# Performance work log

Measured on AMD Instinct MI355X. Metric: run time of the kernel, lower is better.

The kernel has to match this reference:

```python
import jax, jax.numpy as jnp
import numpy as np

B, T, N, DG = 4, 24, 2048, 64
E, H, W, P, NH = 128, 64, 64, 8, 4
HD = E // NH
HP, WP = H // P, W // P
NP = HP * WP
SCALE = float(np.sqrt(HD))


def _mlp(x, w1, b1, w2, b2):
    return jax.nn.relu(x @ w1 + b1) @ w2 + b2


def _interp_linear(x, out_len):
    # x: (B, L, C); linear interpolation along L to out_len, align_corners=False (PyTorch semantics)
    L = x.shape[1]
    src = jnp.maximum((jnp.arange(out_len, dtype=jnp.float32) + 0.5) * (L / out_len) - 0.5, 0.0)
    i0 = jnp.floor(src).astype(jnp.int32)
    lam = (src - i0.astype(jnp.float32))[None, :, None]
    i1 = jnp.minimum(i0 + 1, L - 1)
    return x[:, i0] * (1.0 - lam) + x[:, i1] * lam


def _cross_attn(Q, K, V, qw, qb, kw, kb, vw, vb, ow, ob):
    b, ql, _ = Q.shape
    kl = K.shape[1]
    q = (Q @ qw + qb).reshape(b, ql, NH, HD).transpose(0, 2, 1, 3)
    k = (K @ kw + kb).reshape(b, kl, NH, HD).transpose(0, 2, 1, 3)
    v = (V @ vw + vb).reshape(b, kl, NH, HD).transpose(0, 2, 1, 3)
    s = jnp.einsum('bhqd,bhkd->bhqk', q, k) / SCALE
    a = jax.nn.softmax(s, axis=-1)
    o = jnp.einsum('bhqk,bhkd->bhqd', a, v).transpose(0, 2, 1, 3).reshape(b, ql, E)
    o = o @ ow + ob
    # permute -> F.interpolate(size=k_len, mode='linear') -> permute back
    return _interp_linear(o, kl)


def _forward(graph_features, grid_features, graph_time_indices, grid_time_indices,
             gek_w1, gek_b1, gek_w2, gek_b2, gev_w1, gev_b1, gev_w2, gev_b2,
             rk_w1, rk_b1, rk_w2, rk_b2, rv_w1, rv_b1, rv_w2, rv_b2,
             te_w1, te_b1, te_w2, te_b2, pe_w, pe_b, up_w, up_b,
             ag_q_w, ag_q_b, ag_k_w, ag_k_b, ag_v_w, ag_v_b, ag_o_w, ag_o_b,
             ar_q_w, ar_q_b, ar_k_w, ar_k_b, ar_v_w, ar_v_b, ar_o_w, ar_o_b):
    # time embedding (query), q_len = T
    te = _mlp(graph_time_indices[:, :, None], te_w1, te_b1, te_w2, te_b2)  # (B, T, E)
    # graph branch
    gf = graph_features.reshape(B, T * N, DG)
    gk = _mlp(gf, gek_w1, gek_b1, gek_w2, gek_b2)
    gv = _mlp(gf, gev_w1, gev_b1, gev_w2, gev_b2)
    g_out = _cross_attn(te, gk, gv, ag_q_w, ag_q_b, ag_k_w, ag_k_b, ag_v_w, ag_v_b, ag_o_w, ag_o_b)
    g_out = g_out.reshape(B, T, N, E)
    # grid branch: non-overlapping patch conv (kernel=stride=P) as einsum
    xp = grid_features.reshape(B * T, E, HP, P, WP, P)
    patches = jnp.einsum('bchpwq,ocpq->bhwo', xp, pe_w) + pe_b  # (BT, HP, WP, E)
    patches = patches.reshape(B, T * NP, E)
    rk = _mlp(patches, rk_w1, rk_b1, rk_w2, rk_b2)
    rv = _mlp(patches, rv_w1, rv_b1, rv_w2, rv_b2)
    r_out = _cross_attn(te, rk, rv, ar_q_w, ar_q_b, ar_k_w, ar_k_b, ar_v_w, ar_v_b, ar_o_w, ar_o_b)  # (B, T*NP, E)
    r = r_out.reshape(B * T, HP, WP, E)
    # ConvTranspose2d with kernel=stride=P: each pixel expands to a PxP block
    up = jnp.einsum('bijc,copq->boipjq', r, up_w).reshape(B * T, E, H, W) + up_b[None, :, None, None]
    return g_out, up.reshape(B, T, E, H, W)


def setup_inputs():
    key = jax.random.key(0)
    ks = iter(jax.random.split(key, 64))
    def mk(shape):
        return jax.random.normal(next(ks), shape, dtype=jnp.float32) * 0.02
    d = {}
    d['graph_features'] = jax.random.normal(next(ks), (B, T, N, DG), dtype=jnp.float32)
    d['grid_features'] = jax.random.normal(next(ks), (B, T, E, H, W), dtype=jnp.float32)
    d['graph_time_indices'] = jax.random.uniform(next(ks), (B, T), dtype=jnp.float32)
    d['grid_time_indices'] = jax.random.uniform(next(ks), (B, T), dtype=jnp.float32)
    for pfx, din in (('gek', DG), ('gev', DG), ('rk', E), ('rv', E), ('te', 1)):
        d[pfx + '_w1'] = mk((din, E)); d[pfx + '_b1'] = jnp.zeros((E,), jnp.float32)
        d[pfx + '_w2'] = mk((E, E)); d[pfx + '_b2'] = jnp.zeros((E,), jnp.float32)
    d['pe_w'] = mk((E, E, P, P)); d['pe_b'] = jnp.zeros((E,), jnp.float32)
    d['up_w'] = mk((E, E, P, P)); d['up_b'] = jnp.zeros((E,), jnp.float32)
    for pfx in ('ag', 'ar'):
        for nm in ('q', 'k', 'v', 'o'):
            d[pfx + '_' + nm + '_w'] = mk((E, E)); d[pfx + '_' + nm + '_b'] = jnp.zeros((E,), jnp.float32)
    return d


def reference(graph_features, grid_features, graph_time_indices, grid_time_indices,
              gek_w1, gek_b1, gek_w2, gek_b2, gev_w1, gev_b1, gev_w2, gev_b2,
              rk_w1, rk_b1, rk_w2, rk_b2, rv_w1, rv_b1, rv_w2, rv_b2,
              te_w1, te_b1, te_w2, te_b2, pe_w, pe_b, up_w, up_b,
              ag_q_w, ag_q_b, ag_k_w, ag_k_b, ag_v_w, ag_v_b, ag_o_w, ag_o_b,
              ar_q_w, ar_q_b, ar_k_w, ar_k_b, ar_v_w, ar_v_b, ar_o_w, ar_o_b):
    return _forward(graph_features, grid_features, graph_time_indices, grid_time_indices,
                    gek_w1, gek_b1, gek_w2, gek_b2, gev_w1, gev_b1, gev_w2, gev_b2,
                    rk_w1, rk_b1, rk_w2, rk_b2, rv_w1, rv_b1, rv_w2, rv_b2,
                    te_w1, te_b1, te_w2, te_b2, pe_w, pe_b, up_w, up_b,
                    ag_q_w, ag_q_b, ag_k_w, ag_k_b, ag_v_w, ag_v_b, ag_o_w, ag_o_b,
                    ar_q_w, ar_q_b, ar_k_w, ar_k_b, ar_v_w, ar_v_b, ar_o_w, ar_o_b)
```

## Files before the change

### kernel.cpp

```cpp
#include <hip/hip_runtime.h>


typedef unsigned short u16;
using bf8 = __attribute__((ext_vector_type(8))) short;
using f4v = __attribute__((ext_vector_type(4))) float;
#define MFMA16(a, b, c) __builtin_amdgcn_mfma_f32_16x16x32_bf16(a, b, c, 0, 0, 0)

constexpr float INV_SCALE = 0.17677669529663687f;

__device__ __forceinline__ u16 f2bf(float f) {
  unsigned u = __float_as_uint(f);
  u += 0x7FFFu + ((u >> 16) & 1u);
  return (u16)(u >> 16);
}
__device__ __forceinline__ unsigned pk2(float a, float b) {
  return (unsigned)f2bf(a) | ((unsigned)f2bf(b) << 16);
}
__device__ __forceinline__ float bflo(unsigned v) { return __uint_as_float(v << 16); }
__device__ __forceinline__ float bfhi(unsigned v) { return __uint_as_float(v & 0xffff0000u); }


__global__ __launch_bounds__(128) void k_pre1(
    const float* gk_w1, const float* gv_w1, const float* rk_w1, const float* rv_w1,
    u16* W1c_g, u16* W1c_r,
    const float* pe_w, u16* peB,
    const float* tidx, const float* te_w1, const float* te_b1,
    const float* te_w2, const float* te_b2,
    const float* wg, const float* bg, const float* wr, const float* br,
    float* qg, float* qr,
    const float* A0, const float* Ab0, const float* B0, const float* Bb0, float* O0, float* Ob0,
    const float* A1, const float* Ab1, const float* B1, const float* Bb1, float* O1, float* Ob1,
    const float* A2, const float* Ab2, const float* B2, const float* Bb2, float* O2, float* Ob2,
    const float* A3, const float* Ab3, const float* B3, const float* Bb3, float* O3, float* Ob3) {
  int x = blockIdx.x, e = threadIdx.x;
  __shared__ float sh[256];
  if (x < 512) {
    int c = x & 255, brn = x >> 8;
    int DIN = brn ? 128 : 64;
    if (e < DIN) {
      const float* src = brn ? (c < 128 ? rk_w1 : rv_w1) : (c < 128 ? gk_w1 : gv_w1);
      u16* dst = brn ? W1c_r : W1c_g;
      dst[c * DIN + e] = f2bf(src[e * 128 + (c & 127)]);
    }
  } else if (x < 1536) {
    int i = ((x - 512) * 128 + e) * 8;
    float4 v0 = *(const float4*)(pe_w + i);
    float4 v1 = *(const float4*)(pe_w + i + 4);
    uint4 o; o.x = pk2(v0.x, v0.y); o.y = pk2(v0.z, v0.w);
    o.z = pk2(v1.x, v1.y); o.w = pk2(v1.z, v1.w);
    *(uint4*)&peB[i] = o;
  } else if (x < 1632) {
    int row = x - 1536;
    float tv = tidx[row];
    sh[e] = fmaxf(tv * te_w1[e] + te_b1[e], 0.f);
    __syncthreads();
    float a = te_b2[e];
    for (int j = 0; j < 128; ++j) a += sh[j] * te_w2[j * 128 + e];
    sh[128 + e] = a;
    __syncthreads();
    float ag = bg[e], ar = br[e];
    for (int j = 0; j < 128; ++j) {
      float xx = sh[128 + j];
      ag += xx * wg[j * 128 + e];
      ar += xx * wr[j * 128 + e];
    }
    qg[row * 128 + e] = ag;
    qr[row * 128 + e] = ar;
  } else {
    int sub = x - 1632;
    int task = sub / 129, j = sub % 129;
    const float *A, *Ab, *Bm, *Bb; float *O, *Ob;
    switch (task) {
      case 0: A=A0; Ab=Ab0; Bm=B0; Bb=Bb0; O=O0; Ob=Ob0; break;
      case 1: A=A1; Ab=Ab1; Bm=B1; Bb=Bb1; O=O1; Ob=Ob1; break;
      case 2: A=A2; Ab=Ab2; Bm=B2; Bb=Bb2; O=O2; Ob=Ob2; break;
      default:A=A3; Ab=Ab3; Bm=B3; Bb=Bb3; O=O3; Ob=Ob3; break;
    }
    sh[e] = (j < 128) ? A[j * 128 + e] : Ab[e];
    __syncthreads();
    float acc = (j < 128) ? 0.f : Bb[e];
    for (int m = 0; m < 128; ++m) acc += sh[m] * Bm[m * 128 + e];
    if (j < 128) O[j * 128 + e] = acc; else Ob[e] = acc;
  }
}


__global__ __launch_bounds__(128) void k_wvopk(
    const float* Wv_g, const float* bv_g, const float* ow_g, const float* ob_g, float* Wvo_g, float* bvo_g,
    const float* Wv_r, const float* bv_r, const float* ow_r, const float* ob_r, float* Wvo_r, float* bvo_r,
    const float* Wk_g, const float* bk_g, const float* q_g, u16* PkT_g, float* ck_g,
    const float* Wk_r, const float* bk_r, const float* q_r, u16* PkT_r, float* ck_r) {
  int j = blockIdx.x, e = threadIdx.x;
  if (blockIdx.y < 8) {
    int br = blockIdx.y >> 2, h = blockIdx.y & 3;
    const float* Wv = br ? Wv_r : Wv_g;  const float* bv = br ? bv_r : bv_g;
    const float* ow = br ? ow_r : ow_g;  const float* ob = br ? ob_r : ob_g;
    float* Wvo = br ? Wvo_r : Wvo_g;     float* bvo = br ? bvo_r : bvo_g;
    if (j < 128) {
      __shared__ float wrow[32];
      if (e < 32) wrow[e] = Wv[j * 128 + h * 32 + e];
      __syncthreads();
      float acc = 0.f;
      for (int d = 0; d < 32; ++d) acc += wrow[d] * ow[(h * 32 + d) * 128 + e];
      Wvo[(h * 128 + j) * 128 + e] = acc;
    } else if (h == 0) {
      __shared__ float bbv[128];
      bbv[e] = bv[e];
      __syncthreads();
      float acc = ob[e];
      for (int m = 0; m < 128; ++m) acc += bbv[m] * ow[m * 128 + e];
      bvo[e] = acc;
    }
  } else {
    int y = blockIdx.y - 8;
    int br = y >> 2, b = y & 3;
    int hq = e;
    if (hq >= 96) return;
    const float* Wk = br ? Wk_r : Wk_g;  const float* bk = br ? bk_r : bk_g;
    const float* q  = br ? q_r  : q_g;
    u16* PkT = br ? PkT_r : PkT_g;       float* ck = br ? ck_r : ck_g;
    int h = hq / 24, t = hq % 24;
    const float* qrow = q + (b * 24 + t) * 128 + h * 32;
    if (j < 128) {
      const float* wrow = Wk + j * 128 + h * 32;
      float acc = 0.f;
      for (int d = 0; d < 32; ++d) acc += wrow[d] * qrow[d];
      PkT[((size_t)b * 96 + hq) * 136 + j] = f2bf(acc * INV_SCALE);
    } else {
      float acc = 0.f;
      for (int d = 0; d < 32; ++d) acc += bk[h * 32 + d] * qrow[d];
      ck[b * 96 + hq] = acc * INV_SCALE;
    }
  }
}


template <int DIN, int NRED, bool INBF>
__device__ __forceinline__ void flash_body(char* smem,
    const void* __restrict__ Xv, const float* __restrict__ redbias, size_t rstride,
    const u16* __restrict__ W1c, const float* __restrict__ b1k, const float* __restrict__ b1v,
    const u16* __restrict__ PkT, const float* __restrict__ ck,
    u16* __restrict__ accP, float* __restrict__ lP,
    int KL, int kpb, int chunk, int b, int nchunk) {
  constexpr int KS = DIN / 32;
  constexpr int PD = DIN + 8;
  constexpr int PH = 136, PV = 72, PP = 72;
  constexpr int NR = DIN / 16;
  constexpr int XTN = 64 * PD;
  u16* Xt   = (u16*)smem;
  u16* HB   = (u16*)(smem + 4 * XTN);
  u16* Pt   = (u16*)(smem + 4 * XTN + 18432);
  u16* Pk_s = (u16*)(smem + 4 * XTN + 18432 + 13824);
  float* lred = (float*)(smem + 4 * XTN + 18432 + 13824 + 26112);

  int t = threadIdx.x;
  int l = t & 63, w = t >> 6;
  int l16 = l & 15, l4 = l >> 4;

  size_t xbase = (size_t)b * KL * DIN + (size_t)chunk * kpb * DIN;

  {
    const unsigned* ps = (const unsigned*)(PkT + (size_t)b * 96 * 136);
    unsigned* pd = (unsigned*)Pk_s;
    for (int i = t; i < 96 * 136 / 2; i += 256) pd[i] = ps[i];
  }

  bf8 wkA[2][KS], wvB[2][KS];
#pragma unroll
  for (int m = 0; m < 2; ++m)
#pragma unroll
    for (int ks = 0; ks < KS; ++ks) {
      int hid = w * 32 + m * 16 + l16;
      wkA[m][ks] = *(const bf8*)(W1c + (size_t)hid * DIN + ks * 32 + l4 * 8);
      wvB[m][ks] = *(const bf8*)(W1c + (size_t)(128 + hid) * DIN + ks * 32 + l4 * 8);
    }
  float bkA[2][4], bvB[2], ckr[6];
#pragma unroll
  for (int m = 0; m < 2; ++m)
#pragma unroll
    for (int r = 0; r < 4; ++r) bkA[m][r] = b1k[w * 32 + m * 16 + l4 * 4 + r];
#pragma unroll
  for (int n = 0; n < 2; ++n) bvB[n] = b1v[w * 32 + n * 16 + l16];
#pragma unroll
  for (int n = 0; n < 6; ++n) ckr[n] = ck[b * 96 + n * 16 + l16];

  f4v accO[6][2];
#pragma unroll
  for (int m = 0; m < 6; ++m)
#pragma unroll
    for (int n = 0; n < 2; ++n) accO[m][n] = (f4v){0.f, 0.f, 0.f, 0.f};
  float lacc[6] = {0.f, 0.f, 0.f, 0.f, 0.f, 0.f};

  float4 xr[NR];
  auto load_tile = [&](int kt) {
#pragma unroll
    for (int r = 0; r < NR; ++r) {
      int idx = (r * 256 + t) * 4;
      if constexpr (!INBF) {
        const float* Xrow = (const float*)Xv + xbase + (size_t)kt * 64 * DIN;
        xr[r] = *(const float4*)(Xrow + idx);
      } else {
        const u16* Xrow = (const u16*)Xv + xbase + (size_t)kt * 64 * DIN;
        int din = idx % DIN;
        float4 a = *(const float4*)(redbias + din);
#pragma unroll
        for (int c = 0; c < NRED; ++c) {
          uint2 v = *(const uint2*)(Xrow + (size_t)c * rstride + idx);
          a.x += bflo(v.x); a.y += bfhi(v.x);
          a.z += bflo(v.y); a.w += bfhi(v.y);
        }
        xr[r] = a;
      }
    }
  };

  int ntile = kpb >> 6;
  load_tile(0);
  int buf = 0;
  for (int kt = 0; kt < ntile; ++kt) {
#pragma unroll
    for (int r = 0; r < NR; ++r) {
      int idx = (r * 256 + t) * 4;
      int key = idx / DIN, din = idx % DIN;
      uint2 o; o.x = pk2(xr[r].x, xr[r].y); o.y = pk2(xr[r].z, xr[r].w);
      *(uint2*)&Xt[buf * XTN + key * PD + din] = o;
    }
    if (kt + 1 < ntile) load_tile(kt + 1);
    __syncthreads();

    {
      f4v hk[2][4];
#pragma unroll
      for (int m = 0; m < 2; ++m)
#pragma unroll
        for (int n = 0; n < 4; ++n) hk[m][n] = (f4v){0.f, 0.f, 0.f, 0.f};
#pragma unroll
      for (int ks = 0; ks < KS; ++ks) {
        bf8 xf[4];
#pragma unroll
        for (int n = 0; n < 4; ++n)
          xf[n] = *(const bf8*)&Xt[buf * XTN + (n * 16 + l16) * PD + ks * 32 + l4 * 8];
#pragma unroll
        for (int m = 0; m < 2; ++m)
#pragma unroll
          for (int n = 0; n < 4; ++n) hk[m][n] = MFMA16(wkA[m][ks], xf[n], hk[m][n]);
      }
#pragma unroll
      for (int m = 0; m < 2; ++m)
#pragma unroll
        for (int n = 0; n < 4; ++n) {
          int key = n * 16 + l16;
          int hid0 = w * 32 + m * 16 + l4 * 4;
          float v0 = fmaxf(hk[m][n][0] + bkA[m][0], 0.f);
          float v1 = fmaxf(hk[m][n][1] + bkA[m][1], 0.f);
          float v2 = fmaxf(hk[m][n][2] + bkA[m][2], 0.f);
          float v3 = fmaxf(hk[m][n][3] + bkA[m][3], 0.f);
          uint2 o; o.x = pk2(v0, v1); o.y = pk2(v2, v3);
          *(uint2*)&HB[key * PH + hid0] = o;
        }
    }
    __syncthreads();

    {
      f4v sa[6];
#pragma unroll
      for (int n = 0; n < 6; ++n) sa[n] = (f4v){ckr[n], ckr[n], ckr[n], ckr[n]};
#pragma unroll
      for (int ks = 0; ks < 4; ++ks) {
        bf8 a = *(const bf8*)&HB[(w * 16 + l16) * PH + ks * 32 + l4 * 8];
#pragma unroll
        for (int n = 0; n < 6; ++n) {
          bf8 bp = *(const bf8*)&Pk_s[(n * 16 + l16) * 136 + ks * 32 + l4 * 8];
          sa[n] = MFMA16(a, bp, sa[n]);
        }
      }
#pragma unroll
      for (int n = 0; n < 6; ++n) {
        float e0 = __expf(sa[n][0]), e1 = __expf(sa[n][1]);
        float e2 = __expf(sa[n][2]), e3 = __expf(sa[n][3]);
        float ls = (e0 + e1) + (e2 + e3);
        ls += __shfl_xor(ls, 16);
        ls += __shfl_xor(ls, 32);
        lacc[n] += ls;
        uint2 o; o.x = pk2(e0, e1); o.y = pk2(e2, e3);
        *(uint2*)&Pt[(n * 16 + l16) * PP + w * 16 + l4 * 4] = o;
      }
    }
    __syncthreads();

    {
      f4v hv[4][2];
#pragma unroll
      for (int m = 0; m < 4; ++m)
#pragma unroll
        for (int n = 0; n < 2; ++n) hv[m][n] = (f4v){0.f, 0.f, 0.f, 0.f};
#pragma unroll
      for (int ks = 0; ks < KS; ++ks) {
        bf8 xa[4];
#pragma unroll
        for (int m = 0; m < 4; ++m)
          xa[m] = *(const bf8*)&Xt[buf * XTN + (m * 16 + l16) * PD + ks * 32 + l4 * 8];
#pragma unroll
        for (int m = 0; m < 4; ++m)
#pragma unroll
          for (int n = 0; n < 2; ++n) hv[m][n] = MFMA16(xa[m], wvB[n][ks], hv[m][n]);
      }
#pragma unroll
      for (int m = 0; m < 4; ++m)
#pragma unroll
        for (int n = 0; n < 2; ++n) {
          int d = w * 32 + n * 16 + l16;
          int key0 = m * 16 + l4 * 4;
          float v0 = fmaxf(hv[m][n][0] + bvB[n], 0.f);
          float v1 = fmaxf(hv[m][n][1] + bvB[n], 0.f);
          float v2 = fmaxf(hv[m][n][2] + bvB[n], 0.f);
          float v3 = fmaxf(hv[m][n][3] + bvB[n], 0.f);
          uint2 o; o.x = pk2(v0, v1); o.y = pk2(v2, v3);
          *(uint2*)&HB[d * PV + key0] = o;
        }
    }

#pragma unroll
    for (int ks = 0; ks < 2; ++ks) {
      bf8 pa[6];
#pragma unroll
      for (int m = 0; m < 6; ++m)
        pa[m] = *(const bf8*)&Pt[(m * 16 + l16) * PP + ks * 32 + l4 * 8];
#pragma unroll
      for (int n = 0; n < 2; ++n) {
        bf8 hb = *(const bf8*)&HB[(w * 32 + n * 16 + l16) * PV + ks * 32 + l4 * 8];
#pragma unroll
        for (int m = 0; m < 6; ++m) accO[m][n] = MFMA16(pa[m], hb, accO[m][n]);
      }
    }
    buf ^= 1;
  }

  u16* ap = accP + (size_t)(b * nchunk + chunk) * 96 * 128;
#pragma unroll
  for (int m = 0; m < 6; ++m)
#pragma unroll
    for (int n = 0; n < 2; ++n) {
      int d = w * 32 + n * 16 + l16;
#pragma unroll
      for (int r = 0; r < 4; ++r) {
        int hq = m * 16 + l4 * 4 + r;
        ap[hq * 128 + d] = f2bf(accO[m][n][r]);
      }
    }
  if (l4 == 0) {
#pragma unroll
    for (int n = 0; n < 6; ++n) lred[w * 96 + n * 16 + l16] = lacc[n];
  }
  __syncthreads();
  if (t < 96) {
    float s = lred[t] + lred[96 + t] + lred[192 + t] + lred[288 + t];
    lP[(size_t)(b * nchunk + chunk) * 96 + t] = s;
  }
}


__device__ __forceinline__ void patch_body(char* smem, int bt, int kc,
    const float* __restrict__ X, const u16* __restrict__ peB,
    u16* __restrict__ patchP) {
  u16* Xp = (u16*)smem;
  u16* Wt = (u16*)(smem + 17408);
  int t = threadIdx.x;
  int l = t & 63, w = t >> 6;
  int l16 = l & 15, l4 = l >> 4;
  const float* Xbt = X + (size_t)bt * 524288 + (size_t)kc * 65536;

  f4v acc[4][2];
#pragma unroll
  for (int m = 0; m < 4; ++m)
#pragma unroll
    for (int n = 0; n < 2; ++n) acc[m][n] = (f4v){0.f, 0.f, 0.f, 0.f};

  float4 xr[8];
  auto loadX = [&](int s) {
    const float* img = Xbt + (size_t)s * 8192;
#pragma unroll
    for (int r = 0; r < 8; ++r) xr[r] = *(const float4*)(img + (r * 256 + t) * 4);
  };
  loadX(0);

  for (int s = 0; s < 8; ++s) {
#pragma unroll
    for (int r = 0; r < 8; ++r) {
      int idx = (r * 256 + t) * 4;
      int cl = idx >> 12, off = idx & 4095;
      int h = off >> 6, w0 = off & 63;
      int patch = (h >> 3) * 8 + (w0 >> 3);
      int within = (h & 7) * 8 + (w0 & 7);
      uint2 o; o.x = pk2(xr[r].x, xr[r].y); o.y = pk2(xr[r].z, xr[r].w);
      *(uint2*)&Xp[patch * 136 + cl * 64 + within] = o;
    }
    {
      int colbase = kc * 1024 + s * 128;
#pragma unroll
      for (int r = 0; r < 8; ++r) {
        int idx = r * 256 + t;
        int co = idx >> 4, part = idx & 15;
        int slot = part ^ (co & 7);
        uint4 v = *(const uint4*)(peB + (size_t)co * 8192 + colbase + part * 8);
        *(uint4*)&Wt[co * 128 + slot * 8] = v;
      }
    }
    if (s < 7) loadX(s + 1);
    __syncthreads();
#pragma unroll
    for (int ks2 = 0; ks2 < 4; ++ks2) {
      bf8 af[4];
#pragma unroll
      for (int m = 0; m < 4; ++m)
        af[m] = *(const bf8*)&Xp[(m * 16 + l16) * 136 + ks2 * 32 + l4 * 8];
#pragma unroll
      for (int n = 0; n < 2; ++n) {
        int co = w * 32 + n * 16 + l16;
        int slot = (ks2 * 4 + l4) ^ (co & 7);
        bf8 bf_ = *(const bf8*)&Wt[co * 128 + slot * 8];
#pragma unroll
        for (int m = 0; m < 4; ++m) acc[m][n] = MFMA16(af[m], bf_, acc[m][n]);
      }
    }
    __syncthreads();
  }
  u16* outp = patchP + ((size_t)kc * 6144 + bt * 64) * 128;
#pragma unroll
  for (int m = 0; m < 4; ++m)
#pragma unroll
    for (int n = 0; n < 2; ++n) {
      int d = w * 32 + n * 16 + l16;
#pragma unroll
      for (int r = 0; r < 4; ++r) {
        int patch = m * 16 + l4 * 4 + r;
        outp[patch * 128 + d] = f2bf(acc[m][n][r]);
      }
    }
}


__device__ __forceinline__ void ogred_body(char* smem, int t, int b, int nchunk,
    const u16* __restrict__ accP, const float* __restrict__ lP,
    const float* __restrict__ Wvo, const float* __restrict__ bvo,
    float* __restrict__ og) {
  float* op = (float*)smem;
  float* invl = (float*)(smem + 2048);
  int tid = threadIdx.x;
  for (int p = tid; p < 512; p += 256) {
    int h = p >> 7, e = p & 127;
    const u16* src = accP + ((size_t)b * nchunk * 96 + h * 24 + t) * 128 + e;
    float s = 0.f;
    for (int c = 0; c < nchunk; ++c) s += bflo((unsigned)src[(size_t)c * 12288]);
    op[p] = s;
  }
  if (tid < 4) {
    const float* lp = lP + (size_t)b * nchunk * 96 + tid * 24 + t;
    float ls = 0.f;
    for (int c = 0; c < nchunk; ++c) ls += lp[(size_t)c * 96];
    invl[tid] = 1.f / ls;
  }
  __syncthreads();
  for (int p = tid; p < 512; p += 256) op[p] *= invl[p >> 7];
  __syncthreads();
  if (tid < 128) {
    int e = tid;
    float acc = bvo[e];
    for (int h = 0; h < 4; ++h)
      for (int j = 0; j < 128; ++j) acc += op[h * 128 + j] * Wvo[(h * 128 + j) * 128 + e];
    og[(b * 24 + t) * 128 + e] = acc;
  }
}


__global__ __launch_bounds__(256, 2) void k_big1(
    const float* __restrict__ gf, const u16* __restrict__ W1c_g,
    const float* __restrict__ gek_b1, const float* __restrict__ gev_b1,
    const u16* __restrict__ PkT_g, const float* __restrict__ ck_g,
    u16* __restrict__ accP_g, float* __restrict__ lP_g,
    const float* __restrict__ gridf, const u16* __restrict__ peB,
    u16* __restrict__ patchP) {
  __shared__ __align__(16) char smem[78336];
  int x = blockIdx.x;
  int r5 = x % 5, q5 = x / 5;
  if (r5 < 2) {
    int fid = q5 * 2 + r5;
    flash_body<64, 1, false>(smem, gf, (const float*)nullptr, 0,
        W1c_g, gek_b1, gev_b1, PkT_g, ck_g, accP_g, lP_g,
        49152, 384, fid & 127, fid >> 7, 128);
  } else {
    int pid = q5 * 3 + (r5 - 2);
    patch_body(smem, pid % 96, pid / 96, gridf, peB, patchP);
  }
}


__global__ __launch_bounds__(256, 2) void k_big2(
    const u16* __restrict__ accP_g, const float* __restrict__ lP_g,
    const float* __restrict__ Wvo_g, const float* __restrict__ bvo_g,
    float* __restrict__ og_g,
    const u16* __restrict__ patchP, const float* __restrict__ pe_b,
    const u16* __restrict__ W1c_r,
    const float* __restrict__ rk_b1, const float* __restrict__ rv_b1,
    const u16* __restrict__ PkT_r, const float* __restrict__ ck_r,
    u16* __restrict__ accP_r, float* __restrict__ lP_r) {
  __shared__ __align__(16) char smem[94720];
  int x = blockIdx.x;
  int id = x >> 1;
  if (x & 1) {
    flash_body<128, 8, true>(smem, patchP, pe_b, 786432,
        W1c_r, rk_b1, rv_b1, PkT_r, ck_r, accP_r, lP_r,
        1536, 64, id % 24, id / 24, 24);
  } else {
    ogred_body(smem, id % 24, id / 24, 128, accP_g, lP_g, Wvo_g, bvo_g, og_g);
  }
}


__global__ __launch_bounds__(256) void k_big3(
    const u16* __restrict__ accP_r, const float* __restrict__ lP_r,
    const float* __restrict__ Wvo_r, const float* __restrict__ bvo_r,
    float* __restrict__ og_r,
    const float* __restrict__ og_g, float* __restrict__ outg) {
  __shared__ __align__(16) char smem[2064];
  int x = blockIdx.x;
  if (x < 96) {
    ogred_body(smem, x % 24, x / 24, 24, accP_r, lP_r, Wvo_r, bvo_r, og_r);
  } else {
    int vx = x - 96;
    int b = vx >> 10;
    const float* ogb = og_g + b * 3072;
    float* ob = outg + (size_t)b * 6291456;
    for (int i4 = (vx & 1023) * 256 + threadIdx.x; i4 < 1572864; i4 += 1024 * 256) {
      int i = i4 * 4;
      int n = i >> 7, e = i & 127;
      float src = fmaxf((n + 0.5f) * (1.f / 2048.f) - 0.5f, 0.f);
      int t0 = (int)src; float lam = src - (float)t0; int t1 = min(t0 + 1, 23);
      float4 a = *(const float4*)&ogb[t0 * 128 + e];
      float4 c = *(const float4*)&ogb[t1 * 128 + e];
      float4 o;
      o.x = a.x + lam * (c.x - a.x); o.y = a.y + lam * (c.y - a.y);
      o.z = a.z + lam * (c.z - a.z); o.w = a.w + lam * (c.w - a.w);
      *(float4*)&ob[i] = o;
    }
  }
}


__global__ __launch_bounds__(256) void k_upfuse(const float* __restrict__ og_r,
    const float* __restrict__ up_w, const float* __restrict__ up_b,
    float* __restrict__ outu) {
  int b = blockIdx.x >> 7, o = blockIdx.x & 127;
  __shared__ float og_s[24 * 128];
  __shared__ float upw_s[128 * 64];
  __shared__ float U_s[24 * 64];
  int tid = threadIdx.x;
  for (int i = tid; i < 24 * 128 / 4; i += 256)
    ((float4*)og_s)[i] = ((const float4*)(og_r + b * 3072))[i];
  for (int i = tid; i < 128 * 64 / 4; i += 256) {
    int c = i >> 4, pq4 = i & 15;
    ((float4*)upw_s)[i] = *(const float4*)(up_w + (size_t)c * 8192 + o * 64 + pq4 * 4);
  }
  __syncthreads();
  float bias = up_b[o];
  int pq = tid & 63, tg = tid >> 6;
  float acc[6] = {0.f, 0.f, 0.f, 0.f, 0.f, 0.f};
  for (int c = 0; c < 128; c += 4) {
    float w0 = upw_s[c * 64 + pq], w1 = upw_s[(c + 1) * 64 + pq];
    float w2 = upw_s[(c + 2) * 64 + pq], w3 = upw_s[(c + 3) * 64 + pq];
#pragma unroll
    for (int r = 0; r < 6; ++r) {
      float4 g = *(const float4*)&og_s[(tg * 6 + r) * 128 + c];
      acc[r] += g.x * w0 + g.y * w1 + g.z * w2 + g.w * w3;
    }
  }
#pragma unroll
  for (int r = 0; r < 6; ++r) U_s[(tg * 6 + r) * 64 + pq] = acc[r] + bias;
  __syncthreads();
  for (int i4 = tid; i4 < 24 * 1024; i4 += 256) {
    int i = i4 * 4;
    int t = i >> 12, hw = i & 4095;
    int h = hw >> 6, w0 = hw & 63;
    int ii = h >> 3, p = h & 7, j = w0 >> 3, q0 = w0 & 7;
    int n = t * 64 + ii * 8 + j;
    float src = fmaxf((n + 0.5f) * (1.f / 64.f) - 0.5f, 0.f);
    int t0 = (int)src; float lam = src - (float)t0; int t1 = min(t0 + 1, 23);
    float4 a = *(const float4*)&U_s[t0 * 64 + p * 8 + q0];
    float4 c4 = *(const float4*)&U_s[t1 * 64 + p * 8 + q0];
    float4 r;
    r.x = a.x + lam * (c4.x - a.x); r.y = a.y + lam * (c4.y - a.y);
    r.z = a.z + lam * (c4.z - a.z); r.w = a.w + lam * (c4.w - a.w);
    *(float4*)&outu[((size_t)(b * 24 + t) * 128 + o) * 4096 + hw] = r;
  }
}


extern "C" void kernel_launch(void* const* d_in, const int* in_sizes, int n_in,
                              void* d_out, int out_size, void* d_ws, size_t ws_size,
                              hipStream_t stream) {
  (void)in_sizes; (void)n_in; (void)out_size; (void)ws_size;
  const float* gf    = (const float*)d_in[0];
  const float* gridf = (const float*)d_in[1];
  const float* gti   = (const float*)d_in[2];
  const float* gek_w1 = (const float*)d_in[4],  *gek_b1 = (const float*)d_in[5];
  const float* gek_w2 = (const float*)d_in[6],  *gek_b2 = (const float*)d_in[7];
  const float* gev_w1 = (const float*)d_in[8],  *gev_b1 = (const float*)d_in[9];
  const float* gev_w2 = (const float*)d_in[10], *gev_b2 = (const float*)d_in[11];
  const float* rk_w1  = (const float*)d_in[12], *rk_b1  = (const float*)d_in[13];
  const float* rk_w2  = (const float*)d_in[14], *rk_b2  = (const float*)d_in[15];
  const float* rv_w1  = (const float*)d_in[16], *rv_b1  = (const float*)d_in[17];
  const float* rv_w2  = (const float*)d_in[18], *rv_b2  = (const float*)d_in[19];
  const float* te_w1  = (const float*)d_in[20], *te_b1  = (const float*)d_in[21];
  const float* te_w2  = (const float*)d_in[22], *te_b2  = (const float*)d_in[23];
  const float* pe_w   = (const float*)d_in[24], *pe_b   = (const float*)d_in[25];
  const float* up_w   = (const float*)d_in[26], *up_b   = (const float*)d_in[27];
  const float* ag_q_w = (const float*)d_in[28], *ag_q_b = (const float*)d_in[29];
  const float* ag_k_w = (const float*)d_in[30], *ag_k_b = (const float*)d_in[31];
  const float* ag_v_w = (const float*)d_in[32], *ag_v_b = (const float*)d_in[33];
  const float* ag_o_w = (const float*)d_in[34], *ag_o_b = (const float*)d_in[35];
  const float* ar_q_w = (const float*)d_in[36], *ar_q_b = (const float*)d_in[37];
  const float* ar_k_w = (const float*)d_in[38], *ar_k_b = (const float*)d_in[39];
  const float* ar_v_w = (const float*)d_in[40], *ar_v_b = (const float*)d_in[41];
  const float* ar_o_w = (const float*)d_in[42], *ar_o_b = (const float*)d_in[43];

  float* out = (float*)d_out;
  float* ws = (float*)d_ws;
  size_t off = 0;
  auto A = [&](size_t n) { float* p = ws + off; off += n; return p; };
  float* q_g   = A(12288);   float* q_r   = A(12288);
  float* Wk_g  = A(16384);   float* bk_g  = A(128);
  float* Wv_g  = A(16384);   float* bv_g  = A(128);
  float* Wk_r  = A(16384);   float* bk_r  = A(128);
  float* Wv_r  = A(16384);   float* bv_r  = A(128);
  float* Wvo_g = A(65536);   float* bvo_g = A(128);
  float* Wvo_r = A(65536);   float* bvo_r = A(128);
  float* ck_g  = A(384);     float* ck_r  = A(384);
  u16*   PkT_g = (u16*)A(26112);
  u16*   PkT_r = (u16*)A(26112);
  u16*   W1c_g = (u16*)A(8192);
  u16*   W1c_r = (u16*)A(16384);
  u16*   peB   = (u16*)A(524288);
  float* lP_g  = A(49152);   float* lP_r  = A(9216);
  float* og_g  = A(12288);   float* og_r  = A(12288);
  u16*   accP_g = (u16*)A(3145728);
  u16*   patchP = (u16*)A(3145728);
  u16*   accP_r = (u16*)A(589824);

  k_pre1<<<2148, 128, 0, stream>>>(
      gek_w1, gev_w1, rk_w1, rv_w1, W1c_g, W1c_r,
      pe_w, peB,
      gti, te_w1, te_b1, te_w2, te_b2, ag_q_w, ag_q_b, ar_q_w, ar_q_b, q_g, q_r,
      gek_w2, gek_b2, ag_k_w, ag_k_b, Wk_g, bk_g,
      gev_w2, gev_b2, ag_v_w, ag_v_b, Wv_g, bv_g,
      rk_w2,  rk_b2,  ar_k_w, ar_k_b, Wk_r, bk_r,
      rv_w2,  rv_b2,  ar_v_w, ar_v_b, Wv_r, bv_r);
  k_wvopk<<<dim3(129, 16), 128, 0, stream>>>(
      Wv_g, bv_g, ag_o_w, ag_o_b, Wvo_g, bvo_g,
      Wv_r, bv_r, ar_o_w, ar_o_b, Wvo_r, bvo_r,
      Wk_g, bk_g, q_g, PkT_g, ck_g,
      Wk_r, bk_r, q_r, PkT_r, ck_r);

  k_big1<<<1280, 256, 0, stream>>>(
      gf, W1c_g, gek_b1, gev_b1, PkT_g, ck_g, accP_g, lP_g,
      gridf, peB, patchP);
  k_big2<<<192, 256, 0, stream>>>(
      accP_g, lP_g, Wvo_g, bvo_g, og_g,
      patchP, pe_b, W1c_r, rk_b1, rv_b1, PkT_r, ck_r, accP_r, lP_r);
  k_big3<<<4192, 256, 0, stream>>>(
      accP_r, lP_r, Wvo_r, bvo_r, og_r, og_g, out);
  k_upfuse<<<512, 256, 0, stream>>>(og_r, up_w, up_b, out + 25165824);
}
```

Before: 236.2 us.

## Parallelize partial-reduction body and merge output writer kernels into one launch

The reduction over per-chunk partial attention outputs now uses all 256 threads. Each thread does 16-byte vectorized bf16 loads over a quarter of the chunks, and a shuffle reduction computes the softmax denominators. The Wvo projection is split across two thread halves. The grid-reduction blocks move into their own small kernel, and the two large output-writing stages (upsample and graph interpolation) are fused into one launch so they share the GPU instead of running back to back. This cuts serial per-thread loops and gives the heavy store phases better overlap, at the cost of an extra kernel boundary before the writers.

```diff
diff --git a/kernel.cpp b/kernel.cpp
--- a/kernel.cpp
+++ b/kernel.cpp
@@ -440,36 +440,56 @@
 }
 
 
-__device__ __forceinline__ void ogred_body(char* smem, int t, int b, int nchunk,
+__device__ __forceinline__ void ogred_body(char* smem, int t, int b, int nc,
     const u16* __restrict__ accP, const float* __restrict__ lP,
     const float* __restrict__ Wvo, const float* __restrict__ bvo,
     float* __restrict__ og) {
-  float* op = (float*)smem;
-  float* invl = (float*)(smem + 2048);
+  float* part = (float*)smem;
+  float* invl = part + 2048;
+  float* red  = part + 2052;
   int tid = threadIdx.x;
+  int oct = tid & 15, h = (tid >> 4) & 3, cq = tid >> 6;
+  int cn = nc >> 2;
+  float a8[8];
+#pragma unroll
+  for (int k = 0; k < 8; ++k) a8[k] = 0.f;
+  const u16* base = accP + ((size_t)(b * nc + cq * cn) * 96 + h * 24 + t) * 128 + oct * 8;
+  for (int c = 0; c < cn; ++c) {
+    uint4 v = *(const uint4*)(base + (size_t)c * 12288);
+    a8[0] += bflo(v.x); a8[1] += bfhi(v.x);
+    a8[2] += bflo(v.y); a8[3] += bfhi(v.y);
+    a8[4] += bflo(v.z); a8[5] += bfhi(v.z);
+    a8[6] += bflo(v.w); a8[7] += bfhi(v.w);
+  }
+#pragma unroll
+  for (int k = 0; k < 8; ++k) part[cq * 512 + h * 128 + oct * 8 + k] = a8[k];
+  if (tid < 64) {
+    int hh = tid >> 4, c0 = tid & 15;
+    float ls = 0.f;
+    for (int c = c0; c < nc; c += 16) ls += lP[(size_t)(b * nc + c) * 96 + hh * 24 + t];
+    ls += __shfl_xor(ls, 8); ls += __shfl_xor(ls, 4);
+    ls += __shfl_xor(ls, 2); ls += __shfl_xor(ls, 1);
+    if (c0 == 0) invl[hh] = 1.f / ls;
+  }
+  __syncthreads();
   for (int p = tid; p < 512; p += 256) {
-    int h = p >> 7, e = p & 127;
-    const u16* src = accP + ((size_t)b * nchunk * 96 + h * 24 + t) * 128 + e;
-    float s = 0.f;
-    for (int c = 0; c < nchunk; ++c) s += bflo((unsigned)src[(size_t)c * 12288]);
-    op[p] = s;
-  }
-  if (tid < 4) {
-    const float* lp = lP + (size_t)b * nchunk * 96 + tid * 24 + t;
-    float ls = 0.f;
-    for (int c = 0; c < nchunk; ++c) ls += lp[(size_t)c * 96];
-    invl[tid] = 1.f / ls;
+    float s = (part[p] + part[512 + p]) + (part[1024 + p] + part[1536 + p]);
+    part[p] = s * invl[p >> 7];
   }
   __syncthreads();
-  for (int p = tid; p < 512; p += 256) op[p] *= invl[p >> 7];
+  {
+    int e = tid & 127, jh = tid >> 7;
+    float acc = jh ? 0.f : bvo[e];
+    for (int h2 = 0; h2 < 4; ++h2) {
+      const float* wv = Wvo + (size_t)(h2 * 128 + jh * 64) * 128 + e;
+      const float* o = part + h2 * 128 + jh * 64;
+#pragma unroll 4
+      for (int j = 0; j < 64; ++j) acc += o[j] * wv[(size_t)j * 128];
+    }
+    red[tid] = acc;
+  }
   __syncthreads();
-  if (tid < 128) {
-    int e = tid;
-    float acc = bvo[e];
-    for (int h = 0; h < 4; ++h)
-      for (int j = 0; j < 128; ++j) acc += op[h * 128 + j] * Wvo[(h * 128 + j) * 128 + e];
-    og[(b * 24 + t) * 128 + e] = acc;
-  }
+  if (tid < 128) og[(b * 24 + t) * 128 + tid] = red[tid] + red[128 + tid];
 }
 
 
@@ -517,17 +537,66 @@
 }
 
 
-__global__ __launch_bounds__(256) void k_big3(
+__global__ __launch_bounds__(256) void k_ogr(
     const u16* __restrict__ accP_r, const float* __restrict__ lP_r,
     const float* __restrict__ Wvo_r, const float* __restrict__ bvo_r,
-    float* __restrict__ og_r,
+    float* __restrict__ og_r) {
+  __shared__ __align__(16) char smem[9232];
+  int x = blockIdx.x;
+  ogred_body(smem, x % 24, x / 24, 24, accP_r, lP_r, Wvo_r, bvo_r, og_r);
+}
+
+
+__global__ __launch_bounds__(256) void k_writers(const float* __restrict__ og_r,
+    const float* __restrict__ up_w, const float* __restrict__ up_b,
+    float* __restrict__ outu,
     const float* __restrict__ og_g, float* __restrict__ outg) {
-  __shared__ __align__(16) char smem[2064];
+  __shared__ float og_s[24 * 128];
+  __shared__ float upw_s[128 * 64];
+  __shared__ float U_s[24 * 64];
   int x = blockIdx.x;
-  if (x < 96) {
-    ogred_body(smem, x % 24, x / 24, 24, accP_r, lP_r, Wvo_r, bvo_r, og_r);
+  if (x < 512) {
+    int b = x >> 7, o = x & 127;
+    int tid = threadIdx.x;
+    for (int i = tid; i < 24 * 128 / 4; i += 256)
+      ((float4*)og_s)[i] = ((const float4*)(og_r + b * 3072))[i];
+    for (int i = tid; i < 128 * 64 / 4; i += 256) {
+      int c = i >> 4, pq4 = i & 15;
+      ((float4*)upw_s)[i] = *(const float4*)(up_w + (size_t)c * 8192 + o * 64 + pq4 * 4);
+    }
+    __syncthreads();
+    float bias = up_b[o];
+    int pq = tid & 63, tg = tid >> 6;
+    float acc[6] = {0.f, 0.f, 0.f, 0.f, 0.f, 0.f};
+    for (int c = 0; c < 128; c += 4) {
+      float w0 = upw_s[c * 64 + pq], w1 = upw_s[(c + 1) * 64 + pq];
+      float w2 = upw_s[(c + 2) * 64 + pq], w3 = upw_s[(c + 3) * 64 + pq];
+#pragma unroll
+      for (int r = 0; r < 6; ++r) {
+        float4 g = *(const float4*)&og_s[(tg * 6 + r) * 128 + c];
+        acc[r] += g.x * w0 + g.y * w1 + g.z * w2 + g.w * w3;
+      }
+    }
+#pragma unroll
+    for (int r = 0; r < 6; ++r) U_s[(tg * 6 + r) * 64 + pq] = acc[r] + bias;
+    __syncthreads();
+    for (int i4 = tid; i4 < 24 * 1024; i4 += 256) {
+      int i = i4 * 4;
+      int t = i >> 12, hw = i & 4095;
+      int h = hw >> 6, w0 = hw & 63;
+      int ii = h >> 3, p = h & 7, j = w0 >> 3, q0 = w0 & 7;
+      int n = t * 64 + ii * 8 + j;
+      float src = fmaxf((n + 0.5f) * (1.f / 64.f) - 0.5f, 0.f);
+      int t0 = (int)src; float lam = src - (float)t0; int t1 = min(t0 + 1, 23);
+      float4 a = *(const float4*)&U_s[t0 * 64 + p * 8 + q0];
+      float4 c4 = *(const float4*)&U_s[t1 * 64 + p * 8 + q0];
+      float4 r;
+      r.x = a.x + lam * (c4.x - a.x); r.y = a.y + lam * (c4.y - a.y);
+      r.z = a.z + lam * (c4.z - a.z); r.w = a.w + lam * (c4.w - a.w);
+      *(float4*)&outu[((size_t)(b * 24 + t) * 128 + o) * 4096 + hw] = r;
+    }
   } else {
-    int vx = x - 96;
+    int vx = x - 512;
     int b = vx >> 10;
     const float* ogb = og_g + b * 3072;
     float* ob = outg + (size_t)b * 6291456;
@@ -543,54 +612,6 @@
       o.z = a.z + lam * (c.z - a.z); o.w = a.w + lam * (c.w - a.w);
       *(float4*)&ob[i] = o;
     }
-  }
-}
-
-
-__global__ __launch_bounds__(256) void k_upfuse(const float* __restrict__ og_r,
-    const float* __restrict__ up_w, const float* __restrict__ up_b,
-    float* __restrict__ outu) {
-  int b = blockIdx.x >> 7, o = blockIdx.x & 127;
-  __shared__ float og_s[24 * 128];
-  __shared__ float upw_s[128 * 64];
-  __shared__ float U_s[24 * 64];
-  int tid = threadIdx.x;
-  for (int i = tid; i < 24 * 128 / 4; i += 256)
-    ((float4*)og_s)[i] = ((const float4*)(og_r + b * 3072))[i];
-  for (int i = tid; i < 128 * 64 / 4; i += 256) {
-    int c = i >> 4, pq4 = i & 15;
-    ((float4*)upw_s)[i] = *(const float4*)(up_w + (size_t)c * 8192 + o * 64 + pq4 * 4);
-  }
-  __syncthreads();
-  float bias = up_b[o];
-  int pq = tid & 63, tg = tid >> 6;
-  float acc[6] = {0.f, 0.f, 0.f, 0.f, 0.f, 0.f};
-  for (int c = 0; c < 128; c += 4) {
-    float w0 = upw_s[c * 64 + pq], w1 = upw_s[(c + 1) * 64 + pq];
-    float w2 = upw_s[(c + 2) * 64 + pq], w3 = upw_s[(c + 3) * 64 + pq];
-#pragma unroll
-    for (int r = 0; r < 6; ++r) {
-      float4 g = *(const float4*)&og_s[(tg * 6 + r) * 128 + c];
-      acc[r] += g.x * w0 + g.y * w1 + g.z * w2 + g.w * w3;
-    }
-  }
-#pragma unroll
-  for (int r = 0; r < 6; ++r) U_s[(tg * 6 + r) * 64 + pq] = acc[r] + bias;
-  __syncthreads();
-  for (int i4 = tid; i4 < 24 * 1024; i4 += 256) {
-    int i = i4 * 4;
-    int t = i >> 12, hw = i & 4095;
-    int h = hw >> 6, w0 = hw & 63;
-    int ii = h >> 3, p = h & 7, j = w0 >> 3, q0 = w0 & 7;
-    int n = t * 64 + ii * 8 + j;
-    float src = fmaxf((n + 0.5f) * (1.f / 64.f) - 0.5f, 0.f);
-    int t0 = (int)src; float lam = src - (float)t0; int t1 = min(t0 + 1, 23);
-    float4 a = *(const float4*)&U_s[t0 * 64 + p * 8 + q0];
-    float4 c4 = *(const float4*)&U_s[t1 * 64 + p * 8 + q0];
-    float4 r;
-    r.x = a.x + lam * (c4.x - a.x); r.y = a.y + lam * (c4.y - a.y);
-    r.z = a.z + lam * (c4.z - a.z); r.w = a.w + lam * (c4.w - a.w);
-    *(float4*)&outu[((size_t)(b * 24 + t) * 128 + o) * 4096 + hw] = r;
   }
 }
 
@@ -666,7 +687,6 @@
   k_big2<<<192, 256, 0, stream>>>(
       accP_g, lP_g, Wvo_g, bvo_g, og_g,
       patchP, pe_b, W1c_r, rk_b1, rv_b1, PkT_r, ck_r, accP_r, lP_r);
-  k_big3<<<4192, 256, 0, stream>>>(
-      accP_r, lP_r, Wvo_r, bvo_r, og_r, og_g, out);
-  k_upfuse<<<512, 256, 0, stream>>>(og_r, up_w, up_b, out + 25165824);
-}
+  k_ogr<<<96, 256, 0, stream>>>(accP_r, lP_r, Wvo_r, bvo_r, og_r);
+  k_writers<<<4608, 256, 0, stream>>>(og_r, up_w, up_b, out + 25165824, og_g, out);
+}
```

Result: faster. 213.5 us (-9.6%).
